# Performance work log

Hardware: AMD Instinct MI355X
Metric: run time of the kernel (lower is better)

## Reference

```python
import jax, jax.numpy as jnp
import numpy as np

B, C_IN, HW = 4096, 3, 32
NUM_MODULES, NUM_AGENTS, OUT_DIM = 16, 10, 10
FEAT = 128
HID = 48
BN_EPS = 1e-5


def _conv_block(x, w, b):
    # x: [B,C,H,W], w: [O,I,3,3] -> conv(pad=1) + ReLU + maxpool2
    y = jax.lax.conv_general_dilated(
        x, w, window_strides=(1, 1), padding=((1, 1), (1, 1)),
        dimension_numbers=("NCHW", "OIHW", "NCHW"))
    y = jax.nn.relu(y + b[None, :, None, None])
    return jax.lax.reduce_window(y, -jnp.inf, jax.lax.max,
                                 (1, 1, 2, 2), (1, 1, 2, 2), "VALID")


def setup_inputs() -> dict:
    key = jax.random.key(0)
    ks = jax.random.split(key, 24)

    def lin(k, shape, fan_in):
        return (jax.random.normal(k, shape, dtype=jnp.float32) / np.sqrt(fan_in)).astype(jnp.float32)

    inp = {
        "x": jax.random.normal(ks[0], (B, C_IN, HW, HW), dtype=jnp.float32),
        "tasks": jax.random.randint(ks[1], (B,), 0, NUM_AGENTS, dtype=jnp.int32),
        # conv backbone
        "cw1": lin(ks[2], (32, C_IN, 3, 3), C_IN * 9), "cb1": jnp.zeros((32,), jnp.float32),
        "cw2": lin(ks[3], (32, 32, 3, 3), 32 * 9),     "cb2": jnp.zeros((32,), jnp.float32),
        "cw3": lin(ks[4], (32, 32, 3, 3), 32 * 9),     "cb3": jnp.zeros((32,), jnp.float32),
        "cw4": lin(ks[5], (32, 32, 3, 3), 32 * 9),     "cb4": jnp.zeros((32,), jnp.float32),
        "bn_g": jnp.ones((32,), jnp.float32), "bn_b": jnp.zeros((32,), jnp.float32),
        # routing policies (approx linear policies)
        "wpt": lin(ks[6], (FEAT, NUM_AGENTS), FEAT),                  # per-task assignment (1 agent)
        "wd1": lin(ks[7], (NUM_AGENTS, FEAT, NUM_MODULES), FEAT),    # per-agent decision 1
        "wd2": lin(ks[8], (NUM_AGENTS, HID, NUM_MODULES), HID),      # per-agent decision 2
        "wd3": lin(ks[9], (NUM_AGENTS, HID, NUM_MODULES), HID),      # per-agent decision 3
        # expert banks (stacked Linear layers, stored [in,out])
        "s1_w": lin(ks[10], (NUM_MODULES, FEAT, HID), FEAT), "s1_b": jnp.zeros((NUM_MODULES, HID), jnp.float32),
        "s2_w": lin(ks[11], (NUM_MODULES, HID, HID), HID),   "s2_b": jnp.zeros((NUM_MODULES, HID), jnp.float32),
        "s3_w": lin(ks[12], (NUM_MODULES, HID, OUT_DIM), HID), "s3_b": jnp.zeros((NUM_MODULES, OUT_DIM), jnp.float32),
    }
    return inp


def _decide(feat, wd, agents):
    # gather per-sample agent policy, pick argmax action
    logits = jnp.einsum("bf,bfm->bm", feat, wd[agents])  # [B, num_modules]
    return jnp.argmax(logits, axis=-1)


def _select(feat, w_bank, b_bank, actions, relu=True):
    # per-sample expert gather -> small GEMM -> scatter back (vectorized)
    y = jnp.einsum("bf,bfo->bo", feat, w_bank[actions]) + b_bank[actions]
    return jax.nn.relu(y) if relu else y


def reference(x, tasks, cw1, cb1, cw2, cb2, cw3, cb3, cw4, cb4, bn_g, bn_b,
              wpt, wd1, wd2, wd3, s1_w, s1_b, s2_w, s2_b, s3_w, s3_b):
    y = _conv_block(x, cw1, cb1)
    y = _conv_block(y, cw2, cb2)
    y = _conv_block(y, cw3, cb3)
    y = _conv_block(y, cw4, cb4)
    # BatchNorm2d (training-mode batch stats)
    mu = jnp.mean(y, axis=(0, 2, 3), keepdims=True)
    var = jnp.var(y, axis=(0, 2, 3), keepdims=True)
    y = (y - mu) * jax.lax.rsqrt(var + BN_EPS) * bn_g[None, :, None, None] + bn_b[None, :, None, None]
    y = y.reshape(y.shape[0], -1)  # [B, 128]

    # per-task assignment: single-agent policy picks the agent id per sample
    task_actions = jnp.argmax(y @ wpt, axis=-1)  # [B]

    a1 = _decide(y, wd1, task_actions)
    y = _select(y, s1_w, s1_b, a1, relu=True)
    a2 = _decide(y, wd2, task_actions)
    y = _select(y, s2_w, s2_b, a2, relu=True)
    a3 = _decide(y, wd3, task_actions)
    y = _select(y, s3_w, s3_b, a3, relu=False)
    return y
```

## Files before the change

### kernel.cpp

```cpp
#include <hip/hip_runtime.h>
#include <math.h>


#define IMG_B 4096

typedef _Float16 f16x8 __attribute__((ext_vector_type(8)));
typedef _Float16 f16x4 __attribute__((ext_vector_type(4)));
typedef float    f32x4 __attribute__((ext_vector_type(4)));

__device__ inline f16x8 f16x8_zero() {
    f16x8 z;
    #pragma unroll
    for (int i = 0; i < 8; ++i) z[i] = (_Float16)0.f;
    return z;
}

__global__ __launch_bounds__(256) void twt_kernel(
    const float* __restrict__ cw1, const float* __restrict__ cw2,
    const float* __restrict__ cw3, const float* __restrict__ cw4,
    _Float16* __restrict__ w1s, _Float16* __restrict__ w2s,
    _Float16* __restrict__ w3s, _Float16* __restrict__ w4s)
{
    const int i = blockIdx.x * 256 + threadIdx.x;
    if (i < 2048) {
        const int p = i >> 10, rr = i & 1023;
        const int oc = rr >> 5, k = rr & 31;
        _Float16 val = (_Float16)0.f;
        if (k < 27) {
            float w = cw1[oc * 27 + k];
            _Float16 h = (_Float16)w;
            val = p ? (_Float16)(w - (float)h) : h;
        }
        w1s[p * 1024 + oc * 32 + k] = val;
    }
    if (i < 9216) {
        const int k = i % 9, r = i / 9;
        const int ic2 = r & 31, oc2 = r >> 5;
        {
            float w = cw2[(oc2 * 32 + ic2) * 9 + k];
            _Float16 h = (_Float16)w;
            w2s[(k * 2 + 0) * 1024 + oc2 * 32 + ic2] = h;
            w2s[(k * 2 + 1) * 1024 + oc2 * 32 + ic2] = (_Float16)(w - (float)h);
        }
        {
            float w = cw3[(oc2 * 32 + ic2) * 9 + k];
            _Float16 h = (_Float16)w;
            w3s[(k * 2 + 0) * 1024 + oc2 * 32 + ic2] = h;
            w3s[(k * 2 + 1) * 1024 + oc2 * 32 + ic2] = (_Float16)(w - (float)h);
        }
        {
            float w = cw4[(oc2 * 32 + ic2) * 9 + k];
            _Float16 h = (_Float16)w;
            w4s[(k * 2 + 0) * 1024 + oc2 * 32 + ic2] = h;
            w4s[(k * 2 + 1) * 1024 + oc2 * 32 + ic2] = (_Float16)(w - (float)h);
        }
    }
}

__global__ __launch_bounds__(256, 3) void backbone_kernel(
    const float* __restrict__ x,
    const _Float16* __restrict__ w1s, const float* __restrict__ cb1,
    const _Float16* __restrict__ w2s, const float* __restrict__ cb2,
    const _Float16* __restrict__ w3s, const float* __restrict__ cb3,
    const _Float16* __restrict__ w4s, const float* __restrict__ cb4,
    float* __restrict__ t4)
{
    __shared__ __align__(16) unsigned char smem[50736];
    _Float16* b1h = (_Float16*)smem;
    _Float16* b1l = (_Float16*)(smem + 18432);
    unsigned char* region2 = smem + 36864;
    _Float16* sxh = (_Float16*)region2;
    _Float16* sxl = (_Float16*)(region2 + 6936);
    _Float16* b2h = (_Float16*)region2;
    _Float16* b2l = (_Float16*)(region2 + 4096);
    _Float16* b3h = (_Float16*)(region2 + 8192);
    _Float16* b3l = (_Float16*)(region2 + 10496);
    float*    scr = (float*)region2;

    const int t = threadIdx.x;
    const int b = blockIdx.x;
    const int lane = t & 63;
    const int wv = __builtin_amdgcn_readfirstlane(t >> 6);
    const int xl = lane & 15;
    const int g  = lane >> 4;
    const int aoff = xl * 32 + g * 8;

    {
        unsigned* r2w = (unsigned*)region2;
        for (int i = t; i < 3468; i += 256) r2w[i] = 0;
        for (int i = t; i < 1024; i += 256) {
            const int j = i & 15, cs = (i >> 4) & 1, r = (i >> 5) & 15, P = i >> 9;
            ((unsigned*)(smem + P * 18432))[(r * 18 + (cs ? 17 : 0)) * 16 + j] = 0;
        }
    }
    __syncthreads();

    {
        const float* xb = x + (size_t)b * 3072;
        for (int i = t; i < 3072; i += 256) {
            const int ic = i >> 10, r = i & 1023;
            const float v = xb[i];
            const _Float16 h = (_Float16)v;
            const int o = ic * 1156 + ((r >> 5) + 1) * 34 + (r & 31) + 1;
            sxh[o] = h;
            sxl[o] = (_Float16)(v - (float)h);
        }
    }
    __syncthreads();

    {
        const f16x8 ah0 = *(const f16x8*)(w1s + xl * 32 + g * 8);
        const f16x8 ah1 = *(const f16x8*)(w1s + (16 + xl) * 32 + g * 8);
        const f16x8 al0 = *(const f16x8*)(w1s + 1024 + xl * 32 + g * 8);
        const f16x8 al1 = *(const f16x8*)(w1s + 1024 + (16 + xl) * 32 + g * 8);
        const f32x4 cbias0 = *(const f32x4*)(cb1 + g * 4);
        const f32x4 cbias1 = *(const f32x4*)(cb1 + 16 + g * 4);

        int off_j[8];
        #pragma unroll
        for (int j = 0; j < 8; ++j) {
            int k = g * 8 + j; if (k > 26) k = 26;
            const int ic = k / 9, t9 = k - ic * 9;
            const int dy = t9 / 3, dx = t9 - dy * 3;
            off_j[j] = ic * 1156 + dy * 34 + dx;
        }

        for (int q = 0; q < 4; ++q) {
            const int rp = wv * 4 + q;
            const int y0 = 2 * rp;
            for (int xt = 0; xt < 2; ++xt) {
                const int xpix = xt * 16 + xl;
                f32x4 acc[2][2];
                #pragma unroll
                for (int yy = 0; yy < 2; ++yy)
                    #pragma unroll
                    for (int m = 0; m < 2; ++m)
                        #pragma unroll
                        for (int r = 0; r < 4; ++r) acc[yy][m][r] = 0.f;
                #pragma unroll
                for (int yy = 0; yy < 2; ++yy) {
                    const int base = (y0 + yy) * 34 + xpix;
                    f16x8 bh, bl;
                    #pragma unroll
                    for (int j = 0; j < 8; ++j) {
                        const int o = off_j[j] + base;
                        bh[j] = sxh[o];
                        bl[j] = sxl[o];
                    }
                    acc[yy][0] = __builtin_amdgcn_mfma_f32_16x16x32_f16(ah0, bh, acc[yy][0], 0, 0, 0);
                    acc[yy][0] = __builtin_amdgcn_mfma_f32_16x16x32_f16(ah0, bl, acc[yy][0], 0, 0, 0);
                    acc[yy][0] = __builtin_amdgcn_mfma_f32_16x16x32_f16(al0, bh, acc[yy][0], 0, 0, 0);
                    acc[yy][1] = __builtin_amdgcn_mfma_f32_16x16x32_f16(ah1, bh, acc[yy][1], 0, 0, 0);
                    acc[yy][1] = __builtin_amdgcn_mfma_f32_16x16x32_f16(ah1, bl, acc[yy][1], 0, 0, 0);
                    acc[yy][1] = __builtin_amdgcn_mfma_f32_16x16x32_f16(al1, bh, acc[yy][1], 0, 0, 0);
                }
                #pragma unroll
                for (int m = 0; m < 2; ++m) {
                    f32x4 vv;
                    #pragma unroll
                    for (int r = 0; r < 4; ++r) {
                        float v = fmaxf(acc[0][m][r], acc[1][m][r]);
                        v = fmaxf(v, __shfl_xor(v, 1));
                        vv[r] = fmaxf(v + (m ? cbias1[r] : cbias0[r]), 0.f);
                    }
                    if ((xl & 1) == 0) {
                        const int c = xt * 8 + (xl >> 1) + 1;
                        const int grp = m * 2 + (g >> 1);
                        const int so = (grp + (c >> 1)) & 3;
                        const int e = (rp * 18 + c) * 32 + so * 8 + (g & 1) * 4;
                        f16x4 h4, l4;
                        #pragma unroll
                        for (int r = 0; r < 4; ++r) {
                            const _Float16 h = (_Float16)vv[r];
                            h4[r] = h;
                            l4[r] = (_Float16)(vv[r] - (float)h);
                        }
                        *(f16x4*)(b1h + e) = h4;
                        *(f16x4*)(b1l + e) = l4;
                    }
                }
            }
        }
    }
    __syncthreads();

    {
        for (int i = t; i < 1152; i += 256) ((unsigned*)(region2 + 8192))[i] = 0;

        f32x4 acc[4][2];
        #pragma unroll
        for (int j = 0; j < 4; ++j)
            #pragma unroll
            for (int m = 0; m < 2; ++m)
                #pragma unroll
                for (int r = 0; r < 4; ++r) acc[j][m][r] = 0.f;

        #pragma unroll
        for (int dy = 0; dy < 3; ++dy) {
            #pragma unroll
            for (int dx = 0; dx < 3; ++dx) {
                const _Float16* wb = w2s + (dy * 3 + dx) * 2048;
                const f16x8 ah0 = *(const f16x8*)(wb + aoff);
                const f16x8 ah1 = *(const f16x8*)(wb + 512 + aoff);
                const f16x8 al0 = *(const f16x8*)(wb + 1024 + aoff);
                const f16x8 al1 = *(const f16x8*)(wb + 1536 + aoff);

                const int cxs = xl + dx;
                const int so = (g + (cxs >> 1)) & 3;
                #pragma unroll
                for (int j = 0; j < 4; ++j) {
                    const int sy = 4 * wv + j + dy - 1;
                    if ((unsigned)sy < 16u) {
                        const int e = (sy * 18 + cxs) * 32 + so * 8;
                        const f16x8 bh = *(const f16x8*)(b1h + e);
                        const f16x8 bl = *(const f16x8*)(b1l + e);
                        acc[j][0] = __builtin_amdgcn_mfma_f32_16x16x32_f16(ah0, bh, acc[j][0], 0, 0, 0);
                        acc[j][0] = __builtin_amdgcn_mfma_f32_16x16x32_f16(ah0, bl, acc[j][0], 0, 0, 0);
                        acc[j][0] = __builtin_amdgcn_mfma_f32_16x16x32_f16(al0, bh, acc[j][0], 0, 0, 0);
                        acc[j][1] = __builtin_amdgcn_mfma_f32_16x16x32_f16(ah1, bh, acc[j][1], 0, 0, 0);
                        acc[j][1] = __builtin_amdgcn_mfma_f32_16x16x32_f16(ah1, bl, acc[j][1], 0, 0, 0);
                        acc[j][1] = __builtin_amdgcn_mfma_f32_16x16x32_f16(al1, bh, acc[j][1], 0, 0, 0);
                    }
                }
            }
        }

        const f32x4 bias0 = *(const f32x4*)(cb2 + g * 4);
        const f32x4 bias1 = *(const f32x4*)(cb2 + 16 + g * 4);
        #pragma unroll
        for (int pj = 0; pj < 2; ++pj) {
            #pragma unroll
            for (int m = 0; m < 2; ++m) {
                f32x4 vv;
                #pragma unroll
                for (int r = 0; r < 4; ++r) {
                    float v = fmaxf(acc[2 * pj][m][r], acc[2 * pj + 1][m][r]);
                    v = fmaxf(v, __shfl_xor(v, 1));
                    vv[r] = fmaxf(v + (m ? bias1[r] : bias0[r]), 0.f);
                }
                if ((lane & 1) == 0) {
                    const int pp = (2 * wv + pj) * 8 + (xl >> 1);
                    const int slot = m * 2 + (g >> 1);
                    const int so2 = (slot + (pp >> 1)) & 3;
                    const int e = pp * 32 + so2 * 8 + (g & 1) * 4;
                    f16x4 h4, l4;
                    #pragma unroll
                    for (int r = 0; r < 4; ++r) {
                        const _Float16 h = (_Float16)vv[r];
                        h4[r] = h;
                        l4[r] = (_Float16)(vv[r] - (float)h);
                    }
                    *(f16x4*)(b2h + e) = h4;
                    *(f16x4*)(b2l + e) = l4;
                }
            }
        }
    }
    __syncthreads();

    {
        const int p = wv * 16 + xl;
        const int py3 = p >> 3, px3 = p & 7;
        f32x4 acc[2];
        #pragma unroll
        for (int m = 0; m < 2; ++m)
            #pragma unroll
            for (int r = 0; r < 4; ++r) acc[m][r] = 0.f;

        #pragma unroll
        for (int dy = 0; dy < 3; ++dy) {
            #pragma unroll
            for (int dx = 0; dx < 3; ++dx) {
                const _Float16* wb = w3s + (dy * 3 + dx) * 2048;
                const f16x8 ah0 = *(const f16x8*)(wb + aoff);
                const f16x8 ah1 = *(const f16x8*)(wb + 512 + aoff);
                const f16x8 al0 = *(const f16x8*)(wb + 1024 + aoff);
                const f16x8 al1 = *(const f16x8*)(wb + 1536 + aoff);

                const int syL = py3 + dy - 1, sxL = px3 + dx - 1;
                const bool ok = ((unsigned)syL < 8u) && ((unsigned)sxL < 8u);
                const int cy = syL < 0 ? 0 : (syL > 7 ? 7 : syL);
                const int cx = sxL < 0 ? 0 : (sxL > 7 ? 7 : sxL);
                const int cp = cy * 8 + cx;
                const int so = (g + (cp >> 1)) & 3;
                const int e = cp * 32 + so * 8;
                f16x8 bh = *(const f16x8*)(b2h + e);
                f16x8 bl = *(const f16x8*)(b2l + e);
                if (!ok) { bh = f16x8_zero(); bl = f16x8_zero(); }
                acc[0] = __builtin_amdgcn_mfma_f32_16x16x32_f16(ah0, bh, acc[0], 0, 0, 0);
                acc[0] = __builtin_amdgcn_mfma_f32_16x16x32_f16(ah0, bl, acc[0], 0, 0, 0);
                acc[0] = __builtin_amdgcn_mfma_f32_16x16x32_f16(al0, bh, acc[0], 0, 0, 0);
                acc[1] = __builtin_amdgcn_mfma_f32_16x16x32_f16(ah1, bh, acc[1], 0, 0, 0);
                acc[1] = __builtin_amdgcn_mfma_f32_16x16x32_f16(ah1, bl, acc[1], 0, 0, 0);
                acc[1] = __builtin_amdgcn_mfma_f32_16x16x32_f16(al1, bh, acc[1], 0, 0, 0);
            }
        }

        const f32x4 bias0 = *(const f32x4*)(cb3 + g * 4);
        const f32x4 bias1 = *(const f32x4*)(cb3 + 16 + g * 4);
        #pragma unroll
        for (int m = 0; m < 2; ++m) {
            f32x4 vv;
            #pragma unroll
            for (int r = 0; r < 4; ++r) {
                float v = acc[m][r];
                v = fmaxf(v, __shfl_xor(v, 1));
                v = fmaxf(v, __shfl_xor(v, 8));
                vv[r] = fmaxf(v + (m ? bias1[r] : bias0[r]), 0.f);
            }
            if ((lane & 9) == 0) {
                const int yr = wv;
                const int xr = (xl & 7) >> 1;
                const int pp3 = (yr + 1) * 6 + (xr + 1);
                const int grp = m * 2 + (g >> 1);
                const int so = (grp + (pp3 >> 1)) & 3;
                const int e = pp3 * 32 + so * 8 + (g & 1) * 4;
                f16x4 h4, l4;
                #pragma unroll
                for (int r = 0; r < 4; ++r) {
                    const _Float16 h = (_Float16)vv[r];
                    h4[r] = h;
                    l4[r] = (_Float16)(vv[r] - (float)h);
                }
                *(f16x4*)(b3h + e) = h4;
                *(f16x4*)(b3l + e) = l4;
            }
        }
    }
    __syncthreads();

    {
        f32x4 a4[2];
        #pragma unroll
        for (int m = 0; m < 2; ++m)
            #pragma unroll
            for (int r = 0; r < 4; ++r) a4[m][r] = 0.f;

        for (int t9 = wv; t9 < 9; t9 += 4) {
            const _Float16* wb = w4s + t9 * 2048;
            const f16x8 ah0 = *(const f16x8*)(wb + aoff);
            const f16x8 ah1 = *(const f16x8*)(wb + 512 + aoff);
            const f16x8 al0 = *(const f16x8*)(wb + 1024 + aoff);
            const f16x8 al1 = *(const f16x8*)(wb + 1536 + aoff);
            const int dy = t9 / 3, dx = t9 - dy * 3;
            const int pp3 = ((xl >> 2) + dy) * 6 + (xl & 3) + dx;
            const int so = (g + (pp3 >> 1)) & 3;
            const int e = pp3 * 32 + so * 8;
            const f16x8 bh = *(const f16x8*)(b3h + e);
            const f16x8 bl = *(const f16x8*)(b3l + e);
            a4[0] = __builtin_amdgcn_mfma_f32_16x16x32_f16(ah0, bh, a4[0], 0, 0, 0);
            a4[0] = __builtin_amdgcn_mfma_f32_16x16x32_f16(ah0, bl, a4[0], 0, 0, 0);
            a4[0] = __builtin_amdgcn_mfma_f32_16x16x32_f16(al0, bh, a4[0], 0, 0, 0);
            a4[1] = __builtin_amdgcn_mfma_f32_16x16x32_f16(ah1, bh, a4[1], 0, 0, 0);
            a4[1] = __builtin_amdgcn_mfma_f32_16x16x32_f16(ah1, bl, a4[1], 0, 0, 0);
            a4[1] = __builtin_amdgcn_mfma_f32_16x16x32_f16(al1, bh, a4[1], 0, 0, 0);
        }
        const int off = (wv * 64 + lane) * 8;
        *(f32x4*)(scr + off) = a4[0];
        *(f32x4*)(scr + off + 4) = a4[1];
        __syncthreads();

        f32x4 r0, r1;
        #pragma unroll
        for (int r = 0; r < 4; ++r) { r0[r] = 0.f; r1[r] = 0.f; }
        #pragma unroll
        for (int w = 0; w < 4; ++w) {
            const f32x4 p0 = *(const f32x4*)(scr + (w * 64 + lane) * 8);
            const f32x4 p1 = *(const f32x4*)(scr + (w * 64 + lane) * 8 + 4);
            #pragma unroll
            for (int r = 0; r < 4; ++r) { r0[r] += p0[r]; r1[r] += p1[r]; }
        }
        const f32x4 bias0 = *(const f32x4*)(cb4 + g * 4);
        const f32x4 bias1 = *(const f32x4*)(cb4 + 16 + g * 4);
        const int y = xl >> 2, xx = xl & 3;
        #pragma unroll
        for (int m = 0; m < 2; ++m) {
            f32x4 vv;
            #pragma unroll
            for (int r = 0; r < 4; ++r) {
                float v = m ? r1[r] : r0[r];
                v = fmaxf(v, __shfl_xor(v, 1));
                v = fmaxf(v, __shfl_xor(v, 4));
                vv[r] = fmaxf(v + (m ? bias1[r] : bias0[r]), 0.f);
            }
            if ((xl & 5) == 0) {
                const int oc0 = m * 16 + g * 4;
                #pragma unroll
                for (int r = 0; r < 4; ++r)
                    t4[(size_t)b * 128 + (oc0 + r) * 4 + (y >> 1) * 2 + (xx >> 1)] = vv[r];
            }
        }
    }
}

__global__ __launch_bounds__(256) void bnstats_kernel(
    const float* __restrict__ t4, float* __restrict__ mus, float* __restrict__ rss)
{
    __shared__ double ssum[256];
    __shared__ double ssq[256];
    const int c = blockIdx.x, t = threadIdx.x;
    double s = 0.0, q = 0.0;
    for (int j = t; j < 16384; j += 256) {
        float v = t4[(size_t)(j >> 2) * 128 + c * 4 + (j & 3)];
        s += (double)v;
        q += (double)v * (double)v;
    }
    ssum[t] = s; ssq[t] = q;
    __syncthreads();
    for (int w = 128; w > 0; w >>= 1) {
        if (t < w) { ssum[t] += ssum[t + w]; ssq[t] += ssq[t + w]; }
        __syncthreads();
    }
    if (t == 0) {
        double mu = ssum[0] / 16384.0;
        double var = ssq[0] / 16384.0 - mu * mu;
        mus[c] = (float)mu;
        rss[c] = (float)(1.0 / sqrt(var + 1e-5));
    }
}

__global__ __launch_bounds__(64) void routing_kernel(
    const float* __restrict__ t4, const float* __restrict__ mus,
    const float* __restrict__ rss,
    const float* __restrict__ bng, const float* __restrict__ bnb,
    const float* __restrict__ wpt, const float* __restrict__ wd1,
    const float* __restrict__ wd2, const float* __restrict__ wd3,
    const float* __restrict__ s1w, const float* __restrict__ s1b,
    const float* __restrict__ s2w, const float* __restrict__ s2b,
    const float* __restrict__ s3w, const float* __restrict__ s3b,
    float* __restrict__ out)
{
    __shared__ float f[128];
    __shared__ float h1s[48];
    __shared__ float h2s[48];
    __shared__ float tmp[16];
    __shared__ int act;
    const int t = threadIdx.x, b = blockIdx.x;

    for (int i = t; i < 128; i += 64) {
        int c = i >> 2;
        float v = t4[(size_t)b * 128 + i];
        f[i] = (v - mus[c]) * rss[c] * bng[c] + bnb[c];
    }
    __syncthreads();

    if (t < 10) {
        double a = 0.0;
        for (int k = 0; k < 128; ++k) a = fma((double)f[k], (double)wpt[k * 10 + t], a);
        tmp[t] = (float)a;
    }
    __syncthreads();
    if (t == 0) {
        int bi = 0; float bv = tmp[0];
        for (int i = 1; i < 10; ++i) if (tmp[i] > bv) { bv = tmp[i]; bi = i; }
        act = bi;
    }
    __syncthreads();
    const int agent = act;

    if (t < 16) {
        double a = 0.0;
        const float* w = wd1 + (size_t)agent * 128 * 16 + t;
        for (int k = 0; k < 128; ++k) a = fma((double)f[k], (double)w[k * 16], a);
        tmp[t] = (float)a;
    }
    __syncthreads();
    if (t == 0) {
        int bi = 0; float bv = tmp[0];
        for (int i = 1; i < 16; ++i) if (tmp[i] > bv) { bv = tmp[i]; bi = i; }
        act = bi;
    }
    __syncthreads();
    const int a1 = act;

    if (t < 48) {
        float a = s1b[a1 * 48 + t];
        const float* w = s1w + (size_t)a1 * 128 * 48 + t;
        for (int k = 0; k < 128; ++k) a = fmaf(f[k], w[k * 48], a);
        h1s[t] = fmaxf(a, 0.f);
    }
    __syncthreads();

    if (t < 16) {
        double a = 0.0;
        const float* w = wd2 + (size_t)agent * 48 * 16 + t;
        for (int k = 0; k < 48; ++k) a = fma((double)h1s[k], (double)w[k * 16], a);
        tmp[t] = (float)a;
    }
    __syncthreads();
    if (t == 0) {
        int bi = 0; float bv = tmp[0];
        for (int i = 1; i < 16; ++i) if (tmp[i] > bv) { bv = tmp[i]; bi = i; }
        act = bi;
    }
    __syncthreads();
    const int a2 = act;

    if (t < 48) {
        float a = s2b[a2 * 48 + t];
        const float* w = s2w + (size_t)a2 * 48 * 48 + t;
        for (int k = 0; k < 48; ++k) a = fmaf(h1s[k], w[k * 48], a);
        h2s[t] = fmaxf(a, 0.f);
    }
    __syncthreads();

    if (t < 16) {
        double a = 0.0;
        const float* w = wd3 + (size_t)agent * 48 * 16 + t;
        for (int k = 0; k < 48; ++k) a = fma((double)h2s[k], (double)w[k * 16], a);
        tmp[t] = (float)a;
    }
    __syncthreads();
    if (t == 0) {
        int bi = 0; float bv = tmp[0];
        for (int i = 1; i < 16; ++i) if (tmp[i] > bv) { bv = tmp[i]; bi = i; }
        act = bi;
    }
    __syncthreads();
    const int a3 = act;

    if (t < 10) {
        float a = s3b[a3 * 10 + t];
        const float* w = s3w + (size_t)a3 * 48 * 10 + t;
        for (int k = 0; k < 48; ++k) a = fmaf(h2s[k], w[k * 10], a);
        out[(size_t)b * 10 + t] = a;
    }
}

extern "C" void kernel_launch(void* const* d_in, const int* in_sizes, int n_in,
                              void* d_out, int out_size, void* d_ws, size_t ws_size,
                              hipStream_t stream)
{
    (void)in_sizes; (void)n_in; (void)out_size; (void)ws_size;

    const float* x   = (const float*)d_in[0];
    const float* cw1 = (const float*)d_in[2];
    const float* cb1 = (const float*)d_in[3];
    const float* cw2 = (const float*)d_in[4];
    const float* cb2 = (const float*)d_in[5];
    const float* cw3 = (const float*)d_in[6];
    const float* cb3 = (const float*)d_in[7];
    const float* cw4 = (const float*)d_in[8];
    const float* cb4 = (const float*)d_in[9];
    const float* bng = (const float*)d_in[10];
    const float* bnb = (const float*)d_in[11];
    const float* wpt = (const float*)d_in[12];
    const float* wd1 = (const float*)d_in[13];
    const float* wd2 = (const float*)d_in[14];
    const float* wd3 = (const float*)d_in[15];
    const float* s1w = (const float*)d_in[16];
    const float* s1b = (const float*)d_in[17];
    const float* s2w = (const float*)d_in[18];
    const float* s2b = (const float*)d_in[19];
    const float* s3w = (const float*)d_in[20];
    const float* s3b = (const float*)d_in[21];
    float* out = (float*)d_out;

    float* t4  = (float*)d_ws;
    float* mus = t4 + (size_t)IMG_B * 128;
    float* rss = mus + 32;
    _Float16* w1s = (_Float16*)(rss + 32);
    _Float16* w2s = w1s + 2048;
    _Float16* w3s = w2s + 18432;
    _Float16* w4s = w3s + 18432;

    hipLaunchKernelGGL(twt_kernel, dim3(36), dim3(256), 0, stream,
                       cw1, cw2, cw3, cw4, w1s, w2s, w3s, w4s);
    hipLaunchKernelGGL(backbone_kernel, dim3(IMG_B), dim3(256), 0, stream,
                       x, w1s, cb1, w2s, cb2, w3s, cb3, w4s, cb4, t4);
    hipLaunchKernelGGL(bnstats_kernel, dim3(32), dim3(256), 0, stream, t4, mus, rss);
    hipLaunchKernelGGL(routing_kernel, dim3(IMG_B), dim3(64), 0, stream,
                       t4, mus, rss, bng, bnb, wpt, wd1, wd2, wd3,
                       s1w, s1b, s2w, s2b, s3w, s3b, out);
}
```

Baseline: 189.0 us.

## Use 512-thread backbone blocks and interleave hi/lo input halves in LDS

Doubles the backbone block size from 4 to 8 waves and redistributes conv work: layers 1-2 split output rows across more waves, and layers 3-4 split the two 16-channel output halves across wave pairs. The padded input image is stored as packed hi/lo f16 pairs in one 32-bit word, so each im2col gather needs one LDS read instead of two, with bit-shuffling to rebuild the hi and lo vectors. The aim is more waves per image and fewer LDS loads to hide latency. The cost is more register pressure under the tighter launch bounds (512, 6), and more block-wide syncs spread across more waves.

```diff
diff --git a/kernel.cpp b/kernel.cpp
--- a/kernel.cpp
+++ b/kernel.cpp
@@ -7,6 +7,8 @@
 typedef _Float16 f16x8 __attribute__((ext_vector_type(8)));
 typedef _Float16 f16x4 __attribute__((ext_vector_type(4)));
 typedef float    f32x4 __attribute__((ext_vector_type(4)));
+
+union U16x8 { unsigned u[4]; f16x8 v; };
 
 __device__ inline f16x8 f16x8_zero() {
     f16x8 z;
@@ -57,7 +59,7 @@
     }
 }
 
-__global__ __launch_bounds__(256, 3) void backbone_kernel(
+__global__ __launch_bounds__(512, 6) void backbone_kernel(
     const float* __restrict__ x,
     const _Float16* __restrict__ w1s, const float* __restrict__ cb1,
     const _Float16* __restrict__ w2s, const float* __restrict__ cb2,
@@ -69,8 +71,7 @@
     _Float16* b1h = (_Float16*)smem;
     _Float16* b1l = (_Float16*)(smem + 18432);
     unsigned char* region2 = smem + 36864;
-    _Float16* sxh = (_Float16*)region2;
-    _Float16* sxl = (_Float16*)(region2 + 6936);
+    unsigned* sxu = (unsigned*)region2;
     _Float16* b2h = (_Float16*)region2;
     _Float16* b2l = (_Float16*)(region2 + 4096);
     _Float16* b3h = (_Float16*)(region2 + 8192);
@@ -80,30 +81,30 @@
     const int t = threadIdx.x;
     const int b = blockIdx.x;
     const int lane = t & 63;
-    const int wv = __builtin_amdgcn_readfirstlane(t >> 6);
+    const int w  = __builtin_amdgcn_readfirstlane(t >> 6);
+    const int wr = w >> 1;
+    const int mh = w & 1;
     const int xl = lane & 15;
     const int g  = lane >> 4;
     const int aoff = xl * 32 + g * 8;
 
-    {
-        unsigned* r2w = (unsigned*)region2;
-        for (int i = t; i < 3468; i += 256) r2w[i] = 0;
-        for (int i = t; i < 1024; i += 256) {
-            const int j = i & 15, cs = (i >> 4) & 1, r = (i >> 5) & 15, P = i >> 9;
-            ((unsigned*)(smem + P * 18432))[(r * 18 + (cs ? 17 : 0)) * 16 + j] = 0;
-        }
+    for (int i = t; i < 3468; i += 512) sxu[i] = 0;
+    for (int i = t; i < 1024; i += 512) {
+        const int j = i & 15, cs = (i >> 4) & 1, r = (i >> 5) & 15, P = i >> 9;
+        ((unsigned*)(smem + P * 18432))[(r * 18 + (cs ? 17 : 0)) * 16 + j] = 0;
     }
     __syncthreads();
 
     {
         const float* xb = x + (size_t)b * 3072;
-        for (int i = t; i < 3072; i += 256) {
+        for (int i = t; i < 3072; i += 512) {
             const int ic = i >> 10, r = i & 1023;
             const float v = xb[i];
             const _Float16 h = (_Float16)v;
-            const int o = ic * 1156 + ((r >> 5) + 1) * 34 + (r & 31) + 1;
-            sxh[o] = h;
-            sxl[o] = (_Float16)(v - (float)h);
+            const _Float16 l = (_Float16)(v - (float)h);
+            const unsigned hu = (unsigned)__builtin_bit_cast(unsigned short, h);
+            const unsigned lu = (unsigned)__builtin_bit_cast(unsigned short, l);
+            sxu[ic * 1156 + ((r >> 5) + 1) * 34 + (r & 31) + 1] = hu | (lu << 16);
         }
     }
     __syncthreads();
@@ -125,8 +126,8 @@
             off_j[j] = ic * 1156 + dy * 34 + dx;
         }
 
-        for (int q = 0; q < 4; ++q) {
-            const int rp = wv * 4 + q;
+        for (int q = 0; q < 2; ++q) {
+            const int rp = w * 2 + q;
             const int y0 = 2 * rp;
             for (int xt = 0; xt < 2; ++xt) {
                 const int xpix = xt * 16 + xl;
@@ -140,19 +141,22 @@
                 #pragma unroll
                 for (int yy = 0; yy < 2; ++yy) {
                     const int base = (y0 + yy) * 34 + xpix;
-                    f16x8 bh, bl;
+                    unsigned e[8];
                     #pragma unroll
-                    for (int j = 0; j < 8; ++j) {
-                        const int o = off_j[j] + base;
-                        bh[j] = sxh[o];
-                        bl[j] = sxl[o];
+                    for (int j = 0; j < 8; ++j) e[j] = sxu[off_j[j] + base];
+                    U16x8 Bh, Bl;
+                    #pragma unroll
+                    for (int p = 0; p < 4; ++p) {
+                        const unsigned e0 = e[2 * p], e1 = e[2 * p + 1];
+                        Bh.u[p] = (e0 & 0xffffu) | (e1 << 16);
+                        Bl.u[p] = (e0 >> 16) | (e1 & 0xffff0000u);
                     }
-                    acc[yy][0] = __builtin_amdgcn_mfma_f32_16x16x32_f16(ah0, bh, acc[yy][0], 0, 0, 0);
-                    acc[yy][0] = __builtin_amdgcn_mfma_f32_16x16x32_f16(ah0, bl, acc[yy][0], 0, 0, 0);
-                    acc[yy][0] = __builtin_amdgcn_mfma_f32_16x16x32_f16(al0, bh, acc[yy][0], 0, 0, 0);
-                    acc[yy][1] = __builtin_amdgcn_mfma_f32_16x16x32_f16(ah1, bh, acc[yy][1], 0, 0, 0);
-                    acc[yy][1] = __builtin_amdgcn_mfma_f32_16x16x32_f16(ah1, bl, acc[yy][1], 0, 0, 0);
-                    acc[yy][1] = __builtin_amdgcn_mfma_f32_16x16x32_f16(al1, bh, acc[yy][1], 0, 0, 0);
+                    acc[yy][0] = __builtin_amdgcn_mfma_f32_16x16x32_f16(ah0, Bh.v, acc[yy][0], 0, 0, 0);
+                    acc[yy][0] = __builtin_amdgcn_mfma_f32_16x16x32_f16(ah0, Bl.v, acc[yy][0], 0, 0, 0);
+                    acc[yy][0] = __builtin_amdgcn_mfma_f32_16x16x32_f16(al0, Bh.v, acc[yy][0], 0, 0, 0);
+                    acc[yy][1] = __builtin_amdgcn_mfma_f32_16x16x32_f16(ah1, Bh.v, acc[yy][1], 0, 0, 0);
+                    acc[yy][1] = __builtin_amdgcn_mfma_f32_16x16x32_f16(ah1, Bl.v, acc[yy][1], 0, 0, 0);
+                    acc[yy][1] = __builtin_amdgcn_mfma_f32_16x16x32_f16(al1, Bh.v, acc[yy][1], 0, 0, 0);
                 }
                 #pragma unroll
                 for (int m = 0; m < 2; ++m) {
@@ -185,11 +189,11 @@
     __syncthreads();
 
     {
-        for (int i = t; i < 1152; i += 256) ((unsigned*)(region2 + 8192))[i] = 0;
-
-        f32x4 acc[4][2];
-        #pragma unroll
-        for (int j = 0; j < 4; ++j)
+        for (int i = t; i < 1152; i += 512) ((unsigned*)(region2 + 8192))[i] = 0;
+
+        f32x4 acc[2][2];
+        #pragma unroll
+        for (int j = 0; j < 2; ++j)
             #pragma unroll
             for (int m = 0; m < 2; ++m)
                 #pragma unroll
@@ -208,8 +212,8 @@
                 const int cxs = xl + dx;
                 const int so = (g + (cxs >> 1)) & 3;
                 #pragma unroll
-                for (int j = 0; j < 4; ++j) {
-                    const int sy = 4 * wv + j + dy - 1;
+                for (int j = 0; j < 2; ++j) {
+                    const int sy = 2 * w + j + dy - 1;
                     if ((unsigned)sy < 16u) {
                         const int e = (sy * 18 + cxs) * 32 + so * 8;
                         const f16x8 bh = *(const f16x8*)(b1h + e);
@@ -228,54 +232,47 @@
         const f32x4 bias0 = *(const f32x4*)(cb2 + g * 4);
         const f32x4 bias1 = *(const f32x4*)(cb2 + 16 + g * 4);
         #pragma unroll
-        for (int pj = 0; pj < 2; ++pj) {
-            #pragma unroll
-            for (int m = 0; m < 2; ++m) {
-                f32x4 vv;
+        for (int m = 0; m < 2; ++m) {
+            f32x4 vv;
+            #pragma unroll
+            for (int r = 0; r < 4; ++r) {
+                float v = fmaxf(acc[0][m][r], acc[1][m][r]);
+                v = fmaxf(v, __shfl_xor(v, 1));
+                vv[r] = fmaxf(v + (m ? bias1[r] : bias0[r]), 0.f);
+            }
+            if ((lane & 1) == 0) {
+                const int pp = w * 8 + (xl >> 1);
+                const int slot = m * 2 + (g >> 1);
+                const int so2 = (slot + (pp >> 1)) & 3;
+                const int e = pp * 32 + so2 * 8 + (g & 1) * 4;
+                f16x4 h4, l4;
                 #pragma unroll
                 for (int r = 0; r < 4; ++r) {
-                    float v = fmaxf(acc[2 * pj][m][r], acc[2 * pj + 1][m][r]);
-                    v = fmaxf(v, __shfl_xor(v, 1));
-                    vv[r] = fmaxf(v + (m ? bias1[r] : bias0[r]), 0.f);
+                    const _Float16 h = (_Float16)vv[r];
+                    h4[r] = h;
+                    l4[r] = (_Float16)(vv[r] - (float)h);
                 }
-                if ((lane & 1) == 0) {
-                    const int pp = (2 * wv + pj) * 8 + (xl >> 1);
-                    const int slot = m * 2 + (g >> 1);
-                    const int so2 = (slot + (pp >> 1)) & 3;
-                    const int e = pp * 32 + so2 * 8 + (g & 1) * 4;
-                    f16x4 h4, l4;
-                    #pragma unroll
-                    for (int r = 0; r < 4; ++r) {
-                        const _Float16 h = (_Float16)vv[r];
-                        h4[r] = h;
-                        l4[r] = (_Float16)(vv[r] - (float)h);
-                    }
-                    *(f16x4*)(b2h + e) = h4;
-                    *(f16x4*)(b2l + e) = l4;
-                }
+                *(f16x4*)(b2h + e) = h4;
+                *(f16x4*)(b2l + e) = l4;
             }
         }
     }
     __syncthreads();
 
     {
-        const int p = wv * 16 + xl;
+        const int p = wr * 16 + xl;
         const int py3 = p >> 3, px3 = p & 7;
-        f32x4 acc[2];
-        #pragma unroll
-        for (int m = 0; m < 2; ++m)
-            #pragma unroll
-            for (int r = 0; r < 4; ++r) acc[m][r] = 0.f;
+        f32x4 acc;
+        #pragma unroll
+        for (int r = 0; r < 4; ++r) acc[r] = 0.f;
 
         #pragma unroll
         for (int dy = 0; dy < 3; ++dy) {
             #pragma unroll
             for (int dx = 0; dx < 3; ++dx) {
-                const _Float16* wb = w3s + (dy * 3 + dx) * 2048;
-                const f16x8 ah0 = *(const f16x8*)(wb + aoff);
-                const f16x8 ah1 = *(const f16x8*)(wb + 512 + aoff);
-                const f16x8 al0 = *(const f16x8*)(wb + 1024 + aoff);
-                const f16x8 al1 = *(const f16x8*)(wb + 1536 + aoff);
+                const _Float16* wb = w3s + (dy * 3 + dx) * 2048 + mh * 512;
+                const f16x8 ah = *(const f16x8*)(wb + aoff);
+                const f16x8 al = *(const f16x8*)(wb + 1024 + aoff);
 
                 const int syL = py3 + dy - 1, sxL = px3 + dx - 1;
                 const bool ok = ((unsigned)syL < 8u) && ((unsigned)sxL < 8u);
@@ -287,104 +284,85 @@
                 f16x8 bh = *(const f16x8*)(b2h + e);
                 f16x8 bl = *(const f16x8*)(b2l + e);
                 if (!ok) { bh = f16x8_zero(); bl = f16x8_zero(); }
-                acc[0] = __builtin_amdgcn_mfma_f32_16x16x32_f16(ah0, bh, acc[0], 0, 0, 0);
-                acc[0] = __builtin_amdgcn_mfma_f32_16x16x32_f16(ah0, bl, acc[0], 0, 0, 0);
-                acc[0] = __builtin_amdgcn_mfma_f32_16x16x32_f16(al0, bh, acc[0], 0, 0, 0);
-                acc[1] = __builtin_amdgcn_mfma_f32_16x16x32_f16(ah1, bh, acc[1], 0, 0, 0);
-                acc[1] = __builtin_amdgcn_mfma_f32_16x16x32_f16(ah1, bl, acc[1], 0, 0, 0);
-                acc[1] = __builtin_amdgcn_mfma_f32_16x16x32_f16(al1, bh, acc[1], 0, 0, 0);
-            }
-        }
-
-        const f32x4 bias0 = *(const f32x4*)(cb3 + g * 4);
-        const f32x4 bias1 = *(const f32x4*)(cb3 + 16 + g * 4);
-        #pragma unroll
-        for (int m = 0; m < 2; ++m) {
-            f32x4 vv;
+                acc = __builtin_amdgcn_mfma_f32_16x16x32_f16(ah, bh, acc, 0, 0, 0);
+                acc = __builtin_amdgcn_mfma_f32_16x16x32_f16(ah, bl, acc, 0, 0, 0);
+                acc = __builtin_amdgcn_mfma_f32_16x16x32_f16(al, bh, acc, 0, 0, 0);
+            }
+        }
+
+        const f32x4 bias = *(const f32x4*)(cb3 + mh * 16 + g * 4);
+        f32x4 vv;
+        #pragma unroll
+        for (int r = 0; r < 4; ++r) {
+            float v = acc[r];
+            v = fmaxf(v, __shfl_xor(v, 1));
+            v = fmaxf(v, __shfl_xor(v, 8));
+            vv[r] = fmaxf(v + bias[r], 0.f);
+        }
+        if ((lane & 9) == 0) {
+            const int yr = wr;
+            const int xr = (xl & 7) >> 1;
+            const int pp3 = (yr + 1) * 6 + (xr + 1);
+            const int grp = mh * 2 + (g >> 1);
+            const int so = (grp + (pp3 >> 1)) & 3;
+            const int e = pp3 * 32 + so * 8 + (g & 1) * 4;
+            f16x4 h4, l4;
             #pragma unroll
             for (int r = 0; r < 4; ++r) {
-                float v = acc[m][r];
-                v = fmaxf(v, __shfl_xor(v, 1));
-                v = fmaxf(v, __shfl_xor(v, 8));
-                vv[r] = fmaxf(v + (m ? bias1[r] : bias0[r]), 0.f);
-            }
-            if ((lane & 9) == 0) {
-                const int yr = wv;
-                const int xr = (xl & 7) >> 1;
-                const int pp3 = (yr + 1) * 6 + (xr + 1);
-                const int grp = m * 2 + (g >> 1);
-                const int so = (grp + (pp3 >> 1)) & 3;
-                const int e = pp3 * 32 + so * 8 + (g & 1) * 4;
-                f16x4 h4, l4;
-                #pragma unroll
-                for (int r = 0; r < 4; ++r) {
-                    const _Float16 h = (_Float16)vv[r];
-                    h4[r] = h;
-                    l4[r] = (_Float16)(vv[r] - (float)h);
-                }
-                *(f16x4*)(b3h + e) = h4;
-                *(f16x4*)(b3l + e) = l4;
-            }
+                const _Float16 h = (_Float16)vv[r];
+                h4[r] = h;
+                l4[r] = (_Float16)(vv[r] - (float)h);
+            }
+            *(f16x4*)(b3h + e) = h4;
+            *(f16x4*)(b3l + e) = l4;
         }
     }
     __syncthreads();
 
     {
-        f32x4 a4[2];
-        #pragma unroll
-        for (int m = 0; m < 2; ++m)
-            #pragma unroll
-            for (int r = 0; r < 4; ++r) a4[m][r] = 0.f;
-
-        for (int t9 = wv; t9 < 9; t9 += 4) {
-            const _Float16* wb = w4s + t9 * 2048;
-            const f16x8 ah0 = *(const f16x8*)(wb + aoff);
-            const f16x8 ah1 = *(const f16x8*)(wb + 512 + aoff);
-            const f16x8 al0 = *(const f16x8*)(wb + 1024 + aoff);
-            const f16x8 al1 = *(const f16x8*)(wb + 1536 + aoff);
+        f32x4 a4;
+        #pragma unroll
+        for (int r = 0; r < 4; ++r) a4[r] = 0.f;
+
+        for (int t9 = wr; t9 < 9; t9 += 4) {
+            const _Float16* wb = w4s + t9 * 2048 + mh * 512;
+            const f16x8 ah = *(const f16x8*)(wb + aoff);
+            const f16x8 al = *(const f16x8*)(wb + 1024 + aoff);
             const int dy = t9 / 3, dx = t9 - dy * 3;
             const int pp3 = ((xl >> 2) + dy) * 6 + (xl & 3) + dx;
             const int so = (g + (pp3 >> 1)) & 3;
             const int e = pp3 * 32 + so * 8;
             const f16x8 bh = *(const f16x8*)(b3h + e);
             const f16x8 bl = *(const f16x8*)(b3l + e);
-            a4[0] = __builtin_amdgcn_mfma_f32_16x16x32_f16(ah0, bh, a4[0], 0, 0, 0);
-            a4[0] = __builtin_amdgcn_mfma_f32_16x16x32_f16(ah0, bl, a4[0], 0, 0, 0);
-            a4[0] = __builtin_amdgcn_mfma_f32_16x16x32_f16(al0, bh, a4[0], 0, 0, 0);
-            a4[1] = __builtin_amdgcn_mfma_f32_16x16x32_f16(ah1, bh, a4[1], 0, 0, 0);
-            a4[1] = __builtin_amdgcn_mfma_f32_16x16x32_f16(ah1, bl, a4[1], 0, 0, 0);
-            a4[1] = __builtin_amdgcn_mfma_f32_16x16x32_f16(al1, bh, a4[1], 0, 0, 0);
-        }
-        const int off = (wv * 64 + lane) * 8;
-        *(f32x4*)(scr + off) = a4[0];
-        *(f32x4*)(scr + off + 4) = a4[1];
+            a4 = __builtin_amdgcn_mfma_f32_16x16x32_f16(ah, bh, a4, 0, 0, 0);
+            a4 = __builtin_amdgcn_mfma_f32_16x16x32_f16(ah, bl, a4, 0, 0, 0);
+            a4 = __builtin_amdgcn_mfma_f32_16x16x32_f16(al, bh, a4, 0, 0, 0);
+        }
+        *(f32x4*)(scr + (w * 64 + lane) * 4) = a4;
         __syncthreads();
 
-        f32x4 r0, r1;
-        #pragma unroll
-        for (int r = 0; r < 4; ++r) { r0[r] = 0.f; r1[r] = 0.f; }
-        #pragma unroll
-        for (int w = 0; w < 4; ++w) {
-            const f32x4 p0 = *(const f32x4*)(scr + (w * 64 + lane) * 8);
-            const f32x4 p1 = *(const f32x4*)(scr + (w * 64 + lane) * 8 + 4);
-            #pragma unroll
-            for (int r = 0; r < 4; ++r) { r0[r] += p0[r]; r1[r] += p1[r]; }
-        }
-        const f32x4 bias0 = *(const f32x4*)(cb4 + g * 4);
-        const f32x4 bias1 = *(const f32x4*)(cb4 + 16 + g * 4);
-        const int y = xl >> 2, xx = xl & 3;
-        #pragma unroll
-        for (int m = 0; m < 2; ++m) {
+        if (w < 2) {
+            f32x4 r0;
+            #pragma unroll
+            for (int r = 0; r < 4; ++r) r0[r] = 0.f;
+            #pragma unroll
+            for (int k = 0; k < 4; ++k) {
+                const f32x4 p0 = *(const f32x4*)(scr + ((k * 2 + w) * 64 + lane) * 4);
+                #pragma unroll
+                for (int r = 0; r < 4; ++r) r0[r] += p0[r];
+            }
+            const f32x4 bias = *(const f32x4*)(cb4 + w * 16 + g * 4);
+            const int y = xl >> 2, xx = xl & 3;
             f32x4 vv;
             #pragma unroll
             for (int r = 0; r < 4; ++r) {
-                float v = m ? r1[r] : r0[r];
+                float v = r0[r];
                 v = fmaxf(v, __shfl_xor(v, 1));
                 v = fmaxf(v, __shfl_xor(v, 4));
-                vv[r] = fmaxf(v + (m ? bias1[r] : bias0[r]), 0.f);
+                vv[r] = fmaxf(v + bias[r], 0.f);
             }
             if ((xl & 5) == 0) {
-                const int oc0 = m * 16 + g * 4;
+                const int oc0 = w * 16 + g * 4;
                 #pragma unroll
                 for (int r = 0; r < 4; ++r)
                     t4[(size_t)b * 128 + (oc0 + r) * 4 + (y >> 1) * 2 + (xx >> 1)] = vv[r];
@@ -460,8 +438,8 @@
 
     if (t < 16) {
         double a = 0.0;
-        const float* w = wd1 + (size_t)agent * 128 * 16 + t;
-        for (int k = 0; k < 128; ++k) a = fma((double)f[k], (double)w[k * 16], a);
+        const float* wd = wd1 + (size_t)agent * 128 * 16 + t;
+        for (int k = 0; k < 128; ++k) a = fma((double)f[k], (double)wd[k * 16], a);
         tmp[t] = (float)a;
     }
     __syncthreads();
@@ -475,16 +453,16 @@
 
     if (t < 48) {
         float a = s1b[a1 * 48 + t];
-        const float* w = s1w + (size_t)a1 * 128 * 48 + t;
-        for (int k = 0; k < 128; ++k) a = fmaf(f[k], w[k * 48], a);
+        const float* wd = s1w + (size_t)a1 * 128 * 48 + t;
+        for (int k = 0; k < 128; ++k) a = fmaf(f[k], wd[k * 48], a);
         h1s[t] = fmaxf(a, 0.f);
     }
     __syncthreads();
 
     if (t < 16) {
         double a = 0.0;
-        const float* w = wd2 + (size_t)agent * 48 * 16 + t;
-        for (int k = 0; k < 48; ++k) a = fma((double)h1s[k], (double)w[k * 16], a);
+        const float* wd = wd2 + (size_t)agent * 48 * 16 + t;
+        for (int k = 0; k < 48; ++k) a = fma((double)h1s[k], (double)wd[k * 16], a);
         tmp[t] = (float)a;
     }
     __syncthreads();
@@ -498,16 +476,16 @@
 
     if (t < 48) {
         float a = s2b[a2 * 48 + t];
-        const float* w = s2w + (size_t)a2 * 48 * 48 + t;
-        for (int k = 0; k < 48; ++k) a = fmaf(h1s[k], w[k * 48], a);
+        const float* wd = s2w + (size_t)a2 * 48 * 48 + t;
+        for (int k = 0; k < 48; ++k) a = fmaf(h1s[k], wd[k * 48], a);
         h2s[t] = fmaxf(a, 0.f);
     }
     __syncthreads();
 
     if (t < 16) {
         double a = 0.0;
-        const float* w = wd3 + (size_t)agent * 48 * 16 + t;
-        for (int k = 0; k < 48; ++k) a = fma((double)h2s[k], (double)w[k * 16], a);
+        const float* wd = wd3 + (size_t)agent * 48 * 16 + t;
+        for (int k = 0; k < 48; ++k) a = fma((double)h2s[k], (double)wd[k * 16], a);
         tmp[t] = (float)a;
     }
     __syncthreads();
@@ -521,8 +499,8 @@
 
     if (t < 10) {
         float a = s3b[a3 * 10 + t];
-        const float* w = s3w + (size_t)a3 * 48 * 10 + t;
-        for (int k = 0; k < 48; ++k) a = fmaf(h2s[k], w[k * 10], a);
+        const float* wd = s3w + (size_t)a3 * 48 * 10 + t;
+        for (int k = 0; k < 48; ++k) a = fmaf(h2s[k], wd[k * 10], a);
         out[(size_t)b * 10 + t] = a;
     }
 }
@@ -566,7 +544,7 @@
 
     hipLaunchKernelGGL(twt_kernel, dim3(36), dim3(256), 0, stream,
                        cw1, cw2, cw3, cw4, w1s, w2s, w3s, w4s);
-    hipLaunchKernelGGL(backbone_kernel, dim3(IMG_B), dim3(256), 0, stream,
+    hipLaunchKernelGGL(backbone_kernel, dim3(IMG_B), dim3(512), 0, stream,
                        x, w1s, cb1, w2s, cb2, w3s, cb3, w4s, cb4, t4);
     hipLaunchKernelGGL(bnstats_kernel, dim3(32), dim3(256), 0, stream, t4, mus, rss);
     hipLaunchKernelGGL(routing_kernel, dim3(IMG_B), dim3(64), 0, stream,
```

After: 194.7 us. +3.0%, slower.
